# Kernel optimization log

Hardware: AMD Instinct MI355X
Metric: run time of the kernel (lower is better)

The kernel has to match this reference:

```python
import jax, jax.numpy as jnp
import numpy as np

EPS = 1e-5

def _layernorm(x, g, b):
    m = jnp.mean(x, axis=-1, keepdims=True)
    v = jnp.var(x, axis=-1, keepdims=True)
    return (x - m) * jax.lax.rsqrt(v + EPS) * g + b

def setup_inputs() -> dict:
    key = jax.random.key(0)
    ks = jax.random.split(key, 8)
    B, N, D, H = 4, 2048, 1024, 16
    F = 2 * D
    s = 0.02
    return {
        "x": jax.random.normal(ks[0], (B, N, D), jnp.float32),
        "mask": jnp.zeros((B, N, N), jnp.float32),
        "Wq": jax.random.normal(ks[1], (D, D), jnp.float32) * s,
        "Wk": jax.random.normal(ks[2], (D, D), jnp.float32) * s,
        "Wv": jax.random.normal(ks[3], (D, D), jnp.float32) * s,
        "Wc": jax.random.normal(ks[4], (D, D), jnp.float32) * s,
        "bc": jnp.zeros((D,), jnp.float32),
        "W1": jax.random.normal(ks[5], (D, F), jnp.float32) * s,
        "b1": jnp.zeros((F,), jnp.float32),
        "W2": jax.random.normal(ks[6], (F, D), jnp.float32) * s,
        "b2": jnp.zeros((D,), jnp.float32),
        "g1": jnp.ones((D,), jnp.float32),
        "be1": jnp.zeros((D,), jnp.float32),
        "g2": jnp.ones((D,), jnp.float32),
        "be2": jnp.zeros((D,), jnp.float32),
    }

def reference(x, mask, Wq, Wk, Wv, Wc, bc, W1, b1, W2, b2, g1, be1, g2, be2):
    B, N, D = x.shape
    H = 16
    Dh = D // H
    scale = 1.0 / np.sqrt(Dh).astype(np.float32)
    # projections -> [B, H, N, Dh]
    def heads(t):
        return t.reshape(B, N, H, Dh).transpose(0, 2, 1, 3)
    q = heads(x @ Wq)
    k = heads(x @ Wk)
    v = heads(x @ Wv)
    score = jnp.einsum('bhnd,bhmd->bhnm', q, k) * scale + mask[:, None, :, :]
    attn = jnp.einsum('bhnm,bhmd->bhnd', jax.nn.softmax(score, axis=-1), v)
    attn = attn.transpose(0, 2, 1, 3).reshape(B, N, D)
    x = x + attn @ Wc + bc
    x = _layernorm(x, g1, be1)
    x = x + jnp.maximum(x @ W1 + b1, 0.0) @ W2 + b2
    x = _layernorm(x, g2, be2)
    return x
```

## Files before the change

kernel.cpp:

```cpp
#include <hip/hip_runtime.h>
#include <hip/hip_bf16.h>


#define DEV __device__ __forceinline__

using s16x8  = __attribute__((ext_vector_type(8))) short;
using f32x4  = __attribute__((ext_vector_type(4))) float;

DEV unsigned short f2bf(float f) {
  unsigned u = __float_as_uint(f);
  u += 0x7fffu + ((u >> 16) & 1u);
  return (unsigned short)(u >> 16);
}
DEV unsigned cvt_pk_bf16(float lo, float hi) {
  unsigned r;
  asm("v_cvt_pk_bf16_f32 %0, %1, %2" : "=v"(r) : "v"(lo), "v"(hi));
  return r;
}
DEV float bf2f(unsigned short b) { return __uint_as_float((unsigned)b << 16); }

typedef __attribute__((address_space(3))) unsigned lds_u32_t;
typedef const __attribute__((address_space(1))) unsigned glb_u32_t;

DEV void gld_lds16(const void* g, void* l) {
  __builtin_amdgcn_global_load_lds((glb_u32_t*)g, (lds_u32_t*)l, 16, 0, 0);
}

template<int RELU>
__global__ __launch_bounds__(512, 2)
void gemm8p(const unsigned short* __restrict__ A, const unsigned short* __restrict__ Bt,
            unsigned short* __restrict__ Cb, const float* __restrict__ bias,
            int M, int N, int K)
{
  __shared__ unsigned short Sh[2][2][256 * 64];
  const int tid = threadIdx.x;
  const int w = tid >> 6, lane = tid & 63;
  const int g = lane >> 4, q = lane & 15;
  const int wr = w >> 2, wc = w & 3;

  const int nwg  = gridDim.x * gridDim.y;
  const int flat = blockIdx.y * gridDim.x + blockIdx.x;
  const int rm   = (flat & 7) * (nwg >> 3) + (flat >> 3);
  const int m0 = (rm / gridDim.x) * 256, n0 = (rm % gridDim.x) * 256;

  f32x4 acc[8][4] = {};

  const int srow = w * 8 + (lane >> 3);
  const int scol = ((lane & 7) ^ (lane >> 3)) * 8;
  const unsigned short* Ag = A  + (size_t)(m0 + srow) * K + scol;
  const unsigned short* Bg = Bt + (size_t)(n0 + srow) * K + scol;

  auto STG = [&](const unsigned short* Gb, int buf, int ab, int half, int kt) {
    const unsigned short* gs = Gb + (size_t)(half * 128) * K + kt * 64;
    unsigned short* ls = &Sh[buf][ab][(half * 128 + w * 8) * 64];
    gld_lds16(gs, ls);
    gld_lds16(gs + (size_t)64 * K, ls + 64 * 64);
  };
  auto LDA = [&](int buf, int mq, s16x8 af[4][2]) {
#pragma unroll
    for (int mm = 0; mm < 4; ++mm) {
      const unsigned short* rp = &Sh[buf][0][(wr * 128 + mq * 64 + mm * 16 + q) * 64];
#pragma unroll
      for (int kk = 0; kk < 2; ++kk)
        af[mm][kk] = *(const s16x8*)(rp + (((kk * 4 + g) ^ (q & 7)) * 8));
    }
  };
  auto LDB = [&](int buf, int nq, s16x8 bf[2][2]) {
#pragma unroll
    for (int nn = 0; nn < 2; ++nn) {
      const unsigned short* rp = &Sh[buf][1][(wc * 64 + nq * 32 + nn * 16 + q) * 64];
#pragma unroll
      for (int kk = 0; kk < 2; ++kk)
        bf[nn][kk] = *(const s16x8*)(rp + (((kk * 4 + g) ^ (q & 7)) * 8));
    }
  };
  auto MQ = [&](int mq, int nq, const s16x8 af[4][2], const s16x8 bf[2][2]) {
    __builtin_amdgcn_s_setprio(1);
#pragma unroll
    for (int kk = 0; kk < 2; ++kk)
#pragma unroll
      for (int mm = 0; mm < 4; ++mm)
#pragma unroll
        for (int nn = 0; nn < 2; ++nn)
          acc[mq * 4 + mm][nq * 2 + nn] = __builtin_amdgcn_mfma_f32_16x16x32_bf16(
              af[mm][kk], bf[nn][kk], acc[mq * 4 + mm][nq * 2 + nn], 0, 0, 0);
    __builtin_amdgcn_s_setprio(0);
  };
  auto BAR = [&]() { __builtin_amdgcn_sched_barrier(0); __builtin_amdgcn_s_barrier(); };

  STG(Ag, 0, 0, 0, 0); STG(Ag, 0, 0, 1, 0);
  STG(Bg, 0, 1, 0, 0); STG(Bg, 0, 1, 1, 0);

  const int NKT = K >> 6;
  s16x8 af[4][2], bf0[2][2], bf1[2][2];
#pragma unroll 1
  for (int kt = 0; kt < NKT; ++kt) {
    const int b = kt & 1, sb = b ^ 1, kn = kt + 1;
    const bool stg = (kn < NKT);
    if (stg) { STG(Ag, sb, 0, 0, kn); asm volatile("s_waitcnt vmcnt(2)" ::: "memory"); }
    else     {                        asm volatile("s_waitcnt vmcnt(0)" ::: "memory"); }
    BAR();
    LDA(b, 0, af); LDB(b, 0, bf0);
    MQ(0, 0, af, bf0);
    BAR();
    if (stg) STG(Ag, sb, 0, 1, kn);
    LDB(b, 1, bf1);
    MQ(0, 1, af, bf1);
    BAR();
    if (stg) STG(Bg, sb, 1, 0, kn);
    LDA(b, 1, af);
    MQ(1, 0, af, bf0);
    BAR();
    if (stg) STG(Bg, sb, 1, 1, kn);
    MQ(1, 1, af, bf1);
    BAR();
  }

#pragma unroll
  for (int n = 0; n < 4; ++n) {
    const int col = n0 + wc * 64 + n * 16 + q;
    const float bv = bias ? bias[col] : 0.0f;
#pragma unroll
    for (int m = 0; m < 8; ++m) {
      const int row0 = m0 + wr * 128 + m * 16 + g * 4;
#pragma unroll
      for (int r = 0; r < 4; ++r) {
        float v = acc[m][n][r] + bv;
        if (RELU) v = fmaxf(v, 0.0f);
        Cb[(size_t)(row0 + r) * N + col] = f2bf(v);
      }
    }
  }
}

template<int RELU, int RESID, int OUTF, int VOUT>
__global__ __launch_bounds__(256)
void gemm_bt(const unsigned short* __restrict__ A, const unsigned short* __restrict__ Bt,
             unsigned short* __restrict__ Cb, float* __restrict__ Cf,
             const float* __restrict__ bias, const float* __restrict__ resid,
             const unsigned short* __restrict__ residb,
             unsigned short* __restrict__ vtout,
             int M, int N, int K)
{
  __shared__ unsigned short As[2][4096];
  __shared__ unsigned short Bs[2][4096];
  const int tid  = threadIdx.x;
  const int wave = tid >> 6, lane = tid & 63;
  const int g = lane >> 4, q = lane & 15;

  const int nwg  = gridDim.x * gridDim.y;
  const int flat = blockIdx.y * gridDim.x + blockIdx.x;
  const int rm   = (nwg & 7) ? flat : ((flat & 7) * (nwg >> 3) + (flat >> 3));
  const int m0 = (rm / gridDim.x) * 128, n0 = (rm % gridDim.x) * 128;
  const int wr = wave >> 1, wc = wave & 1;

  f32x4 acc[4][4] = {};

  const int i0 = wave * 512 + lane * 8;
  const int i1 = 2048 + i0;

  auto STAGE = [&](int buf, int kt) {
    gld_lds16(A  + (size_t)(m0 + (i0 >> 5)) * K + kt + (i0 & 31), As[buf] + wave * 512);
    gld_lds16(Bt + (size_t)(n0 + (i0 >> 5)) * K + kt + (i0 & 31), Bs[buf] + wave * 512);
    gld_lds16(A  + (size_t)(m0 + (i1 >> 5)) * K + kt + (i1 & 31), As[buf] + 2048 + wave * 512);
    gld_lds16(Bt + (size_t)(n0 + (i1 >> 5)) * K + kt + (i1 & 31), Bs[buf] + 2048 + wave * 512);
  };

  STAGE(0, 0);
  __syncthreads();
  int cur = 0;
#pragma unroll 1
  for (int kt = 0; kt < K; kt += 32) {
    if (kt + 32 < K) STAGE(cur ^ 1, kt + 32);
    s16x8 a[4], b[4];
#pragma unroll
    for (int m = 0; m < 4; ++m)
      a[m] = *(const s16x8*)(As[cur] + (wr * 64 + m * 16 + q) * 32 + g * 8);
#pragma unroll
    for (int n = 0; n < 4; ++n)
      b[n] = *(const s16x8*)(Bs[cur] + (wc * 64 + n * 16 + q) * 32 + g * 8);
    __builtin_amdgcn_s_setprio(1);
#pragma unroll
    for (int m = 0; m < 4; ++m)
#pragma unroll
      for (int n = 0; n < 4; ++n)
        acc[m][n] = __builtin_amdgcn_mfma_f32_16x16x32_bf16(a[m], b[n], acc[m][n], 0, 0, 0);
    __builtin_amdgcn_s_setprio(0);
    __syncthreads();
    cur ^= 1;
  }

#pragma unroll
  for (int n = 0; n < 4; ++n) {
    const int col = n0 + wc * 64 + n * 16 + q;
    if (VOUT && col >= 2048) {
      const int cv = col - 2048;
#pragma unroll
      for (int m = 0; m < 4; ++m) {
        const int row0 = m0 + wr * 64 + m * 16 + g * 4;
        const int bb = row0 >> 11;
        ushort4 pk;
        pk.x = f2bf(acc[m][n][0]); pk.y = f2bf(acc[m][n][1]);
        pk.z = f2bf(acc[m][n][2]); pk.w = f2bf(acc[m][n][3]);
        *(ushort4*)(vtout + ((size_t)bb * 1024 + cv) * 2048 + (row0 & 2047)) = pk;
      }
    } else {
      const float scl = (VOUT && col < 1024) ? 0.18033688011112042f : 1.0f;
      const float bv = bias ? bias[col] : 0.0f;
#pragma unroll
      for (int m = 0; m < 4; ++m) {
        const int row0 = m0 + wr * 64 + m * 16 + g * 4;
#pragma unroll
        for (int r = 0; r < 4; ++r) {
          float v = VOUT ? (acc[m][n][r] * scl) : (acc[m][n][r] + bv);
          if (RELU) v = fmaxf(v, 0.0f);
          if (RESID == 1) v += resid[(size_t)(row0 + r) * N + col];
          if (RESID == 2) v += bf2f(residb[(size_t)(row0 + r) * N + col]);
          if (OUTF) Cf[(size_t)(row0 + r) * N + col] = v;
          else      Cb[(size_t)(row0 + r) * N + col] = f2bf(v);
        }
      }
    }
  }
}

__global__ __launch_bounds__(256)
void mcast_kernel(const float* __restrict__ in, unsigned short* __restrict__ out)
{
  const size_t i = ((size_t)blockIdx.x * 256 + threadIdx.x) * 4;
  const f32x4 v = *(const f32x4*)(in + i);
  const float L2E = 1.4426950408889634f;
  uint2 pk;
  pk.x = cvt_pk_bf16(fmaf(v[0], L2E, -8.0f), fmaf(v[1], L2E, -8.0f));
  pk.y = cvt_pk_bf16(fmaf(v[2], L2E, -8.0f), fmaf(v[3], L2E, -8.0f));
  *(uint2*)(out + i) = pk;
}

__global__ __launch_bounds__(256, 4)
void attn_kernel(const unsigned short* __restrict__ qkv,
                 const unsigned short* __restrict__ vt,
                 const unsigned short* __restrict__ mkb,
                 unsigned short* __restrict__ outb)
{
  __shared__ unsigned short Ks[2][4096];
  __shared__ unsigned short Vs[2][4096];
  __shared__ unsigned short Pl[4][1024];
  const int tid = threadIdx.x, wave = tid >> 6, lane = tid & 63;
  const int g = lane >> 4, q = lane & 15;

  const int flat = blockIdx.y * 32 + blockIdx.x;
  const int rm   = (flat & 7) * 256 + (flat >> 3);
  const int qt = rm & 31, bh = rm >> 5;
  const int b = bh >> 4, h = bh & 15;
  const int qrow = qt * 64 + wave * 16;
  const size_t tok0 = (size_t)b * 2048;

  const unsigned short* Qp = qkv + (tok0 + qrow + q) * 3072 + h * 64;
  const s16x8 bq0 = *(const s16x8*)(Qp + g * 8);
  const s16x8 bq1 = *(const s16x8*)(Qp + 32 + g * 8);
  const unsigned short* Mb = mkb + ((size_t)b * 2048 + qrow + q) * 2048 + g * 4;

  const int lr = lane >> 3;
  const int sc = (lane & 7) ^ lr;
  const unsigned short* Kg = qkv + tok0 * 3072 + 1024 + h * 64
                           + (size_t)(wave * 16 + lr) * 3072 + sc * 8;
  const unsigned short* Vg = vt + ((size_t)bh * 64 + wave * 16 + lr) * 2048 + sc * 8;
  unsigned short* KsW = Ks[0] + wave * 1024;
  unsigned short* VsW = Vs[0] + wave * 1024;

  s16x8 ones;
#pragma unroll
  for (int j = 0; j < 8; ++j) ones[j] = (short)0x3F80;

  f32x4 ot[4] = {};
  f32x4 sacc = {};
  f32x4 mk0[4], mk1[4];
  char* Pw = (char*)&Pl[wave][0];

  gld_lds16(Kg,            KsW);
  gld_lds16(Kg + 8 * 3072, KsW + 512);
  gld_lds16(Vg,            VsW);
  gld_lds16(Vg + 8 * 2048, VsW + 512);
#pragma unroll
  for (int m2 = 0; m2 < 4; ++m2) {
    const uint2 u = *(const uint2*)(Mb + m2 * 16);
    mk0[m2][0] = __uint_as_float(u.x << 16);
    mk0[m2][1] = __uint_as_float(u.x & 0xffff0000u);
    mk0[m2][2] = __uint_as_float(u.y << 16);
    mk0[m2][3] = __uint_as_float(u.y & 0xffff0000u);
  }
  __syncthreads();

#define ATTN_TILE(BUF, MKC, MKN, STG)                                          \
  {                                                                            \
    uint2 mu[4];                                                               \
    if (STG) {                                                                 \
      Kg += 64 * 3072; Vg += 64; Mb += 64;                                     \
      gld_lds16(Kg,            KsW + (BUF ^ 1) * 4096);                        \
      gld_lds16(Kg + 8 * 3072, KsW + (BUF ^ 1) * 4096 + 512);                  \
      gld_lds16(Vg,            VsW + (BUF ^ 1) * 4096);                        \
      gld_lds16(Vg + 8 * 2048, VsW + (BUF ^ 1) * 4096 + 512);                  \
      mu[0] = *(const uint2*)(Mb);      mu[1] = *(const uint2*)(Mb + 16);      \
      mu[2] = *(const uint2*)(Mb + 32); mu[3] = *(const uint2*)(Mb + 48);      \
    }                                                                          \
    f32x4 st[4];                                                               \
    _Pragma("unroll")                                                          \
    for (int m2 = 0; m2 < 4; ++m2) st[m2] = MKC[m2];                           \
    __builtin_amdgcn_s_setprio(1);                                             \
    _Pragma("unroll")                                                          \
    for (int m2 = 0; m2 < 4; ++m2) {                                           \
      const unsigned short* kp = Ks[BUF] + (m2 * 16 + q) * 64;                 \
      const s16x8 ak0 = *(const s16x8*)(kp + ((g       ^ (q & 7)) * 8));       \
      const s16x8 ak1 = *(const s16x8*)(kp + (((g + 4) ^ (q & 7)) * 8));       \
      st[m2] = __builtin_amdgcn_mfma_f32_16x16x32_bf16(ak0, bq0, st[m2], 0, 0, 0); \
      st[m2] = __builtin_amdgcn_mfma_f32_16x16x32_bf16(ak1, bq1, st[m2], 0, 0, 0); \
    }                                                                          \
    __builtin_amdgcn_s_setprio(0);                                             \
    _Pragma("unroll")                                                          \
    for (int m2 = 0; m2 < 4; ++m2) {                                           \
      st[m2][0] = exp2f(st[m2][0]); st[m2][1] = exp2f(st[m2][1]);              \
      st[m2][2] = exp2f(st[m2][2]); st[m2][3] = exp2f(st[m2][3]);              \
      const int bir  = m2 * 32 + g * 8;                                        \
      const int addr = q * 128 + (((bir >> 4) ^ (q & 7)) << 4) + (bir & 15);   \
      uint2 pk;                                                                \
      pk.x = cvt_pk_bf16(st[m2][0], st[m2][1]);                                \
      pk.y = cvt_pk_bf16(st[m2][2], st[m2][3]);                                \
      *(uint2*)(Pw + addr) = pk;                                               \
    }                                                                          \
    __builtin_amdgcn_s_setprio(1);                                             \
    _Pragma("unroll")                                                          \
    for (int kb = 0; kb < 2; ++kb) {                                           \
      const int blk = (kb * 4 + g) ^ (q & 7);                                  \
      const s16x8 pb = *(const s16x8*)(Pw + q * 128 + blk * 16);               \
      sacc = __builtin_amdgcn_mfma_f32_16x16x32_bf16(ones, pb, sacc, 0, 0, 0); \
      _Pragma("unroll")                                                        \
      for (int mm = 0; mm < 4; ++mm) {                                         \
        const s16x8 av = *(const s16x8*)(Vs[BUF] + (mm * 16 + q) * 64 + blk * 8); \
        ot[mm] = __builtin_amdgcn_mfma_f32_16x16x32_bf16(av, pb, ot[mm], 0, 0, 0); \
      }                                                                        \
    }                                                                          \
    __builtin_amdgcn_s_setprio(0);                                             \
    if (STG) {                                                                 \
      _Pragma("unroll")                                                        \
      for (int m2 = 0; m2 < 4; ++m2) {                                         \
        MKN[m2][0] = __uint_as_float(mu[m2].x << 16);                          \
        MKN[m2][1] = __uint_as_float(mu[m2].x & 0xffff0000u);                  \
        MKN[m2][2] = __uint_as_float(mu[m2].y << 16);                          \
        MKN[m2][3] = __uint_as_float(mu[m2].y & 0xffff0000u);                  \
      }                                                                        \
    }                                                                          \
    __syncthreads();                                                           \
  }

#pragma unroll 1
  for (int tt = 0; tt < 16; ++tt) {
    ATTN_TILE(0, mk0, mk1, true);
    ATTN_TILE(1, mk1, mk0, (tt < 15));
  }
#undef ATTN_TILE

  const float inv = 1.0f / sacc[0];
#pragma unroll
  for (int mm = 0; mm < 4; ++mm) {
    const int bir  = mm * 32 + g * 8;
    const int addr = q * 128 + (((bir >> 4) ^ (q & 7)) << 4) + (bir & 15);
    uint2 pk;
    pk.x = cvt_pk_bf16(ot[mm][0] * inv, ot[mm][1] * inv);
    pk.y = cvt_pk_bf16(ot[mm][2] * inv, ot[mm][3] * inv);
    *(uint2*)(Pw + addr) = pk;
  }
#pragma unroll
  for (int p = 0; p < 2; ++p) {
    const int c  = p * 64 + lane;
    const int qq = c >> 3, cc = c & 7;
    const int blk = cc ^ (qq & 7);
    const s16x8 vv = *(const s16x8*)(Pw + qq * 128 + blk * 16);
    *(s16x8*)(outb + (tok0 + qrow + qq) * 1024 + h * 64 + cc * 8) = vv;
  }
}

template<int INBF>
__global__ __launch_bounds__(256)
void ln_kernel(const float* __restrict__ inf, const unsigned short* __restrict__ inb,
               float* __restrict__ outf, unsigned short* __restrict__ outb,
               const float* __restrict__ gam, const float* __restrict__ bet)
{
  __shared__ float red[8];
  const int row = blockIdx.x, tid = threadIdx.x;
  f32x4 v;
  if (INBF) {
    const uint2 u = *(const uint2*)(inb + (size_t)row * 1024 + tid * 4);
    v[0] = __uint_as_float(u.x << 16); v[1] = __uint_as_float(u.x & 0xffff0000u);
    v[2] = __uint_as_float(u.y << 16); v[3] = __uint_as_float(u.y & 0xffff0000u);
  } else {
    v = *(const f32x4*)(inf + (size_t)row * 1024 + tid * 4);
  }
  float s  = v[0] + v[1] + v[2] + v[3];
  float ss = v[0]*v[0] + v[1]*v[1] + v[2]*v[2] + v[3]*v[3];
#pragma unroll
  for (int o = 1; o < 64; o <<= 1) { s += __shfl_xor(s, o); ss += __shfl_xor(ss, o); }
  if ((tid & 63) == 0) { red[tid >> 6] = s; red[4 + (tid >> 6)] = ss; }
  __syncthreads();
  s  = red[0] + red[1] + red[2] + red[3];
  ss = red[4] + red[5] + red[6] + red[7];
  const float mean = s * (1.0f / 1024.0f);
  const float var  = ss * (1.0f / 1024.0f) - mean * mean;
  const float rstd = rsqrtf(var + 1e-5f);
  const f32x4 gm = *(const f32x4*)(gam + tid * 4);
  const f32x4 bt = *(const f32x4*)(bet + tid * 4);
  f32x4 o;
#pragma unroll
  for (int j = 0; j < 4; ++j) o[j] = (v[j] - mean) * rstd * gm[j] + bt[j];
  if (outf) *(f32x4*)(outf + (size_t)row * 1024 + tid * 4) = o;
  if (outb) {
    uint2 pk; pk.x = cvt_pk_bf16(o[0], o[1]); pk.y = cvt_pk_bf16(o[2], o[3]);
    *(uint2*)(outb + (size_t)row * 1024 + tid * 4) = pk;
  }
}

__global__ __launch_bounds__(256)
void tcast_kernel(const float* __restrict__ in, unsigned short* __restrict__ out, int R, int C)
{
  __shared__ float t[32][33];
  const int tx = threadIdx.x & 31, ty = threadIdx.x >> 5;
  const int c0 = blockIdx.x * 32, r0 = blockIdx.y * 32;
#pragma unroll
  for (int k = 0; k < 4; ++k)
    t[ty + k * 8][tx] = in[(size_t)(r0 + ty + k * 8) * C + c0 + tx];
  __syncthreads();
#pragma unroll
  for (int k = 0; k < 4; ++k)
    out[(size_t)(c0 + ty + k * 8) * R + r0 + tx] = f2bf(t[tx][ty + k * 8]);
}

__global__ __launch_bounds__(256)
void cast_x_kernel(const float* __restrict__ in, unsigned short* __restrict__ out)
{
  const size_t i = ((size_t)blockIdx.x * 256 + threadIdx.x) * 4;
  const f32x4 v = *(const f32x4*)(in + i);
  uint2 pk; pk.x = cvt_pk_bf16(v[0], v[1]); pk.y = cvt_pk_bf16(v[2], v[3]);
  *(uint2*)(out + i) = pk;
}

extern "C" void kernel_launch(void* const* d_in, const int* in_sizes, int n_in,
                              void* d_out, int out_size, void* d_ws, size_t ws_size,
                              hipStream_t stream)
{
  (void)in_sizes; (void)n_in; (void)out_size; (void)ws_size;
  const float* x   = (const float*)d_in[0];
  const float* msk = (const float*)d_in[1];
  const float* Wq  = (const float*)d_in[2];
  const float* Wk  = (const float*)d_in[3];
  const float* Wv  = (const float*)d_in[4];
  const float* Wc  = (const float*)d_in[5];
  const float* bc  = (const float*)d_in[6];
  const float* W1  = (const float*)d_in[7];
  const float* b1  = (const float*)d_in[8];
  const float* W2  = (const float*)d_in[9];
  const float* b2  = (const float*)d_in[10];
  const float* g1  = (const float*)d_in[11];
  const float* be1 = (const float*)d_in[12];
  const float* g2  = (const float*)d_in[13];
  const float* be2 = (const float*)d_in[14];
  float* out = (float*)d_out;
  char* ws = (char*)d_ws;
  const size_t MB = 1u << 20;
  unsigned short* xb    = (unsigned short*)(ws + 0 * MB);
  unsigned short* wqkvt = (unsigned short*)(ws + 16 * MB);
  unsigned short* wct   = (unsigned short*)(ws + 22 * MB);
  unsigned short* w1t   = (unsigned short*)(ws + 24 * MB);
  unsigned short* w2t   = (unsigned short*)(ws + 28 * MB);
  unsigned short* qkv   = (unsigned short*)(ws + 32 * MB);
  unsigned short* vt    = (unsigned short*)(ws + 80 * MB);
  unsigned short* attnb = (unsigned short*)(ws + 96 * MB);
  unsigned short* mkb   = (unsigned short*)(ws + 112 * MB);
  unsigned short* y1b   = (unsigned short*)(ws + 112 * MB);
  unsigned short* h1b   = (unsigned short*)(ws + 128 * MB);
  unsigned short* midb  = (unsigned short*)(ws + 32 * MB);
  unsigned short* z2b   = (unsigned short*)(ws + 64 * MB);

  cast_x_kernel<<<8192, 256, 0, stream>>>(x, xb);
  mcast_kernel<<<16384, 256, 0, stream>>>(msk, mkb);
  tcast_kernel<<<dim3(32, 32), 256, 0, stream>>>(Wq, wqkvt,               1024, 1024);
  tcast_kernel<<<dim3(32, 32), 256, 0, stream>>>(Wk, wqkvt + 1024 * 1024, 1024, 1024);
  tcast_kernel<<<dim3(32, 32), 256, 0, stream>>>(Wv, wqkvt + 2048 * 1024, 1024, 1024);
  tcast_kernel<<<dim3(32, 32), 256, 0, stream>>>(Wc, wct,                 1024, 1024);
  tcast_kernel<<<dim3(64, 32), 256, 0, stream>>>(W1, w1t,                 1024, 2048);
  tcast_kernel<<<dim3(32, 64), 256, 0, stream>>>(W2, w2t,                 2048, 1024);

  gemm_bt<0, 0, 0, 1><<<dim3(24, 64), 256, 0, stream>>>(xb, wqkvt, qkv, nullptr,
                                                        nullptr, nullptr, nullptr, vt,
                                                        8192, 3072, 1024);
  attn_kernel<<<dim3(32, 64), 256, 0, stream>>>(qkv, vt, mkb, attnb);
  gemm_bt<0, 2, 0, 0><<<dim3(8, 64), 256, 0, stream>>>(attnb, wct, y1b, nullptr,
                                                       bc, nullptr, xb, nullptr,
                                                       8192, 1024, 1024);
  ln_kernel<1><<<8192, 256, 0, stream>>>(nullptr, y1b, nullptr, h1b, g1, be1);
  gemm8p<1><<<dim3(8, 32), 512, 0, stream>>>(h1b, w1t, midb, b1, 8192, 2048, 1024);
  gemm_bt<0, 2, 0, 0><<<dim3(8, 64), 256, 0, stream>>>(midb, w2t, z2b, nullptr,
                                                       b2, nullptr, h1b, nullptr,
                                                       8192, 1024, 2048);
  ln_kernel<1><<<8192, 256, 0, stream>>>(nullptr, z2b, out, nullptr, g2, be2);
}
```

Before: 422.4 us.

## Move QKV projection to 256-tile GEMM and fuse mask conversion into attention

The QKV projection moves from the 128x128 gemm_bt kernel to the larger 256x256 gemm8p kernel, which gains a VOUT path for writing transposed V and scaling Q. The separate mask-to-bf16 cast kernel is removed. The attention kernel now reads the fp32 mask directly and applies the log2e scale and offset inline. The QK accumulator is initialised in place from the mask registers instead of a copy. This drops one launch and a 32MB intermediate write and read, but the attention kernel now reads twice the mask bytes per tile, which may raise its memory pressure.

```diff
diff --git a/kernel.cpp b/kernel.cpp
--- a/kernel.cpp
+++ b/kernel.cpp
@@ -26,11 +26,11 @@
   __builtin_amdgcn_global_load_lds((glb_u32_t*)g, (lds_u32_t*)l, 16, 0, 0);
 }
 
-template<int RELU>
+template<int RELU, int VOUT>
 __global__ __launch_bounds__(512, 2)
 void gemm8p(const unsigned short* __restrict__ A, const unsigned short* __restrict__ Bt,
             unsigned short* __restrict__ Cb, const float* __restrict__ bias,
-            int M, int N, int K)
+            unsigned short* __restrict__ vtout, int M, int N, int K)
 {
   __shared__ unsigned short Sh[2][2][256 * 64];
   const int tid = threadIdx.x;
@@ -119,85 +119,11 @@
 #pragma unroll
   for (int n = 0; n < 4; ++n) {
     const int col = n0 + wc * 64 + n * 16 + q;
-    const float bv = bias ? bias[col] : 0.0f;
-#pragma unroll
-    for (int m = 0; m < 8; ++m) {
-      const int row0 = m0 + wr * 128 + m * 16 + g * 4;
-#pragma unroll
-      for (int r = 0; r < 4; ++r) {
-        float v = acc[m][n][r] + bv;
-        if (RELU) v = fmaxf(v, 0.0f);
-        Cb[(size_t)(row0 + r) * N + col] = f2bf(v);
-      }
-    }
-  }
-}
-
-template<int RELU, int RESID, int OUTF, int VOUT>
-__global__ __launch_bounds__(256)
-void gemm_bt(const unsigned short* __restrict__ A, const unsigned short* __restrict__ Bt,
-             unsigned short* __restrict__ Cb, float* __restrict__ Cf,
-             const float* __restrict__ bias, const float* __restrict__ resid,
-             const unsigned short* __restrict__ residb,
-             unsigned short* __restrict__ vtout,
-             int M, int N, int K)
-{
-  __shared__ unsigned short As[2][4096];
-  __shared__ unsigned short Bs[2][4096];
-  const int tid  = threadIdx.x;
-  const int wave = tid >> 6, lane = tid & 63;
-  const int g = lane >> 4, q = lane & 15;
-
-  const int nwg  = gridDim.x * gridDim.y;
-  const int flat = blockIdx.y * gridDim.x + blockIdx.x;
-  const int rm   = (nwg & 7) ? flat : ((flat & 7) * (nwg >> 3) + (flat >> 3));
-  const int m0 = (rm / gridDim.x) * 128, n0 = (rm % gridDim.x) * 128;
-  const int wr = wave >> 1, wc = wave & 1;
-
-  f32x4 acc[4][4] = {};
-
-  const int i0 = wave * 512 + lane * 8;
-  const int i1 = 2048 + i0;
-
-  auto STAGE = [&](int buf, int kt) {
-    gld_lds16(A  + (size_t)(m0 + (i0 >> 5)) * K + kt + (i0 & 31), As[buf] + wave * 512);
-    gld_lds16(Bt + (size_t)(n0 + (i0 >> 5)) * K + kt + (i0 & 31), Bs[buf] + wave * 512);
-    gld_lds16(A  + (size_t)(m0 + (i1 >> 5)) * K + kt + (i1 & 31), As[buf] + 2048 + wave * 512);
-    gld_lds16(Bt + (size_t)(n0 + (i1 >> 5)) * K + kt + (i1 & 31), Bs[buf] + 2048 + wave * 512);
-  };
-
-  STAGE(0, 0);
-  __syncthreads();
-  int cur = 0;
-#pragma unroll 1
-  for (int kt = 0; kt < K; kt += 32) {
-    if (kt + 32 < K) STAGE(cur ^ 1, kt + 32);
-    s16x8 a[4], b[4];
-#pragma unroll
-    for (int m = 0; m < 4; ++m)
-      a[m] = *(const s16x8*)(As[cur] + (wr * 64 + m * 16 + q) * 32 + g * 8);
-#pragma unroll
-    for (int n = 0; n < 4; ++n)
-      b[n] = *(const s16x8*)(Bs[cur] + (wc * 64 + n * 16 + q) * 32 + g * 8);
-    __builtin_amdgcn_s_setprio(1);
-#pragma unroll
-    for (int m = 0; m < 4; ++m)
-#pragma unroll
-      for (int n = 0; n < 4; ++n)
-        acc[m][n] = __builtin_amdgcn_mfma_f32_16x16x32_bf16(a[m], b[n], acc[m][n], 0, 0, 0);
-    __builtin_amdgcn_s_setprio(0);
-    __syncthreads();
-    cur ^= 1;
-  }
-
-#pragma unroll
-  for (int n = 0; n < 4; ++n) {
-    const int col = n0 + wc * 64 + n * 16 + q;
     if (VOUT && col >= 2048) {
       const int cv = col - 2048;
 #pragma unroll
-      for (int m = 0; m < 4; ++m) {
-        const int row0 = m0 + wr * 64 + m * 16 + g * 4;
+      for (int m = 0; m < 8; ++m) {
+        const int row0 = m0 + wr * 128 + m * 16 + g * 4;
         const int bb = row0 >> 11;
         ushort4 pk;
         pk.x = f2bf(acc[m][n][0]); pk.y = f2bf(acc[m][n][1]);
@@ -208,38 +134,99 @@
       const float scl = (VOUT && col < 1024) ? 0.18033688011112042f : 1.0f;
       const float bv = bias ? bias[col] : 0.0f;
 #pragma unroll
-      for (int m = 0; m < 4; ++m) {
-        const int row0 = m0 + wr * 64 + m * 16 + g * 4;
+      for (int m = 0; m < 8; ++m) {
+        const int row0 = m0 + wr * 128 + m * 16 + g * 4;
 #pragma unroll
         for (int r = 0; r < 4; ++r) {
-          float v = VOUT ? (acc[m][n][r] * scl) : (acc[m][n][r] + bv);
+          float v = acc[m][n][r] * scl + bv;
           if (RELU) v = fmaxf(v, 0.0f);
-          if (RESID == 1) v += resid[(size_t)(row0 + r) * N + col];
-          if (RESID == 2) v += bf2f(residb[(size_t)(row0 + r) * N + col]);
-          if (OUTF) Cf[(size_t)(row0 + r) * N + col] = v;
-          else      Cb[(size_t)(row0 + r) * N + col] = f2bf(v);
+          Cb[(size_t)(row0 + r) * N + col] = f2bf(v);
         }
       }
     }
   }
 }
 
+template<int RELU, int RESID, int OUTF>
 __global__ __launch_bounds__(256)
-void mcast_kernel(const float* __restrict__ in, unsigned short* __restrict__ out)
-{
-  const size_t i = ((size_t)blockIdx.x * 256 + threadIdx.x) * 4;
-  const f32x4 v = *(const f32x4*)(in + i);
-  const float L2E = 1.4426950408889634f;
-  uint2 pk;
-  pk.x = cvt_pk_bf16(fmaf(v[0], L2E, -8.0f), fmaf(v[1], L2E, -8.0f));
-  pk.y = cvt_pk_bf16(fmaf(v[2], L2E, -8.0f), fmaf(v[3], L2E, -8.0f));
-  *(uint2*)(out + i) = pk;
+void gemm_bt(const unsigned short* __restrict__ A, const unsigned short* __restrict__ Bt,
+             unsigned short* __restrict__ Cb, float* __restrict__ Cf,
+             const float* __restrict__ bias, const float* __restrict__ resid,
+             const unsigned short* __restrict__ residb,
+             int M, int N, int K)
+{
+  __shared__ unsigned short As[2][4096];
+  __shared__ unsigned short Bs[2][4096];
+  const int tid  = threadIdx.x;
+  const int wave = tid >> 6, lane = tid & 63;
+  const int g = lane >> 4, q = lane & 15;
+
+  const int nwg  = gridDim.x * gridDim.y;
+  const int flat = blockIdx.y * gridDim.x + blockIdx.x;
+  const int rm   = (nwg & 7) ? flat : ((flat & 7) * (nwg >> 3) + (flat >> 3));
+  const int m0 = (rm / gridDim.x) * 128, n0 = (rm % gridDim.x) * 128;
+  const int wr = wave >> 1, wc = wave & 1;
+
+  f32x4 acc[4][4] = {};
+
+  const int i0 = wave * 512 + lane * 8;
+  const int i1 = 2048 + i0;
+
+  auto STAGE = [&](int buf, int kt) {
+    gld_lds16(A  + (size_t)(m0 + (i0 >> 5)) * K + kt + (i0 & 31), As[buf] + wave * 512);
+    gld_lds16(Bt + (size_t)(n0 + (i0 >> 5)) * K + kt + (i0 & 31), Bs[buf] + wave * 512);
+    gld_lds16(A  + (size_t)(m0 + (i1 >> 5)) * K + kt + (i1 & 31), As[buf] + 2048 + wave * 512);
+    gld_lds16(Bt + (size_t)(n0 + (i1 >> 5)) * K + kt + (i1 & 31), Bs[buf] + 2048 + wave * 512);
+  };
+
+  STAGE(0, 0);
+  __syncthreads();
+  int cur = 0;
+#pragma unroll 1
+  for (int kt = 0; kt < K; kt += 32) {
+    if (kt + 32 < K) STAGE(cur ^ 1, kt + 32);
+    s16x8 a[4], b[4];
+#pragma unroll
+    for (int m = 0; m < 4; ++m)
+      a[m] = *(const s16x8*)(As[cur] + (wr * 64 + m * 16 + q) * 32 + g * 8);
+#pragma unroll
+    for (int n = 0; n < 4; ++n)
+      b[n] = *(const s16x8*)(Bs[cur] + (wc * 64 + n * 16 + q) * 32 + g * 8);
+    __builtin_amdgcn_s_setprio(1);
+#pragma unroll
+    for (int m = 0; m < 4; ++m)
+#pragma unroll
+      for (int n = 0; n < 4; ++n)
+        acc[m][n] = __builtin_amdgcn_mfma_f32_16x16x32_bf16(a[m], b[n], acc[m][n], 0, 0, 0);
+    __builtin_amdgcn_s_setprio(0);
+    __syncthreads();
+    cur ^= 1;
+  }
+
+#pragma unroll
+  for (int n = 0; n < 4; ++n) {
+    const int col = n0 + wc * 64 + n * 16 + q;
+    const float bv = bias ? bias[col] : 0.0f;
+#pragma unroll
+    for (int m = 0; m < 4; ++m) {
+      const int row0 = m0 + wr * 64 + m * 16 + g * 4;
+#pragma unroll
+      for (int r = 0; r < 4; ++r) {
+        float v = acc[m][n][r] + bv;
+        if (RELU) v = fmaxf(v, 0.0f);
+        if (RESID == 1) v += resid[(size_t)(row0 + r) * N + col];
+        if (RESID == 2) v += bf2f(residb[(size_t)(row0 + r) * N + col]);
+        if (OUTF) Cf[(size_t)(row0 + r) * N + col] = v;
+        else      Cb[(size_t)(row0 + r) * N + col] = f2bf(v);
+      }
+    }
+  }
 }
 
 __global__ __launch_bounds__(256, 4)
 void attn_kernel(const unsigned short* __restrict__ qkv,
                  const unsigned short* __restrict__ vt,
-                 const unsigned short* __restrict__ mkb,
+                 const float* __restrict__ mask,
                  unsigned short* __restrict__ outb)
 {
   __shared__ unsigned short Ks[2][4096];
@@ -258,7 +245,7 @@
   const unsigned short* Qp = qkv + (tok0 + qrow + q) * 3072 + h * 64;
   const s16x8 bq0 = *(const s16x8*)(Qp + g * 8);
   const s16x8 bq1 = *(const s16x8*)(Qp + 32 + g * 8);
-  const unsigned short* Mb = mkb + ((size_t)b * 2048 + qrow + q) * 2048 + g * 4;
+  const float* Mp = mask + ((size_t)b * 2048 + qrow + q) * 2048 + g * 4;
 
   const int lr = lane >> 3;
   const int sc = (lane & 7) ^ lr;
@@ -276,6 +263,7 @@
   f32x4 sacc = {};
   f32x4 mk0[4], mk1[4];
   char* Pw = (char*)&Pl[wave][0];
+  const float L2E = 1.4426950408889634f;
 
   gld_lds16(Kg,            KsW);
   gld_lds16(Kg + 8 * 3072, KsW + 512);
@@ -283,48 +271,43 @@
   gld_lds16(Vg + 8 * 2048, VsW + 512);
 #pragma unroll
   for (int m2 = 0; m2 < 4; ++m2) {
-    const uint2 u = *(const uint2*)(Mb + m2 * 16);
-    mk0[m2][0] = __uint_as_float(u.x << 16);
-    mk0[m2][1] = __uint_as_float(u.x & 0xffff0000u);
-    mk0[m2][2] = __uint_as_float(u.y << 16);
-    mk0[m2][3] = __uint_as_float(u.y & 0xffff0000u);
+    const f32x4 r = *(const f32x4*)(Mp + m2 * 16);
+#pragma unroll
+    for (int i = 0; i < 4; ++i) mk0[m2][i] = fmaf(r[i], L2E, -8.0f);
   }
   __syncthreads();
 
 #define ATTN_TILE(BUF, MKC, MKN, STG)                                          \
   {                                                                            \
-    uint2 mu[4];                                                               \
+    f32x4 mu[4];                                                               \
     if (STG) {                                                                 \
-      Kg += 64 * 3072; Vg += 64; Mb += 64;                                     \
+      Kg += 64 * 3072; Vg += 64; Mp += 64;                                     \
       gld_lds16(Kg,            KsW + (BUF ^ 1) * 4096);                        \
       gld_lds16(Kg + 8 * 3072, KsW + (BUF ^ 1) * 4096 + 512);                  \
       gld_lds16(Vg,            VsW + (BUF ^ 1) * 4096);                        \
       gld_lds16(Vg + 8 * 2048, VsW + (BUF ^ 1) * 4096 + 512);                  \
-      mu[0] = *(const uint2*)(Mb);      mu[1] = *(const uint2*)(Mb + 16);      \
-      mu[2] = *(const uint2*)(Mb + 32); mu[3] = *(const uint2*)(Mb + 48);      \
+      mu[0] = *(const f32x4*)(Mp);      mu[1] = *(const f32x4*)(Mp + 16);      \
+      mu[2] = *(const f32x4*)(Mp + 32); mu[3] = *(const f32x4*)(Mp + 48);      \
     }                                                                          \
-    f32x4 st[4];                                                               \
-    _Pragma("unroll")                                                          \
-    for (int m2 = 0; m2 < 4; ++m2) st[m2] = MKC[m2];                           \
     __builtin_amdgcn_s_setprio(1);                                             \
     _Pragma("unroll")                                                          \
     for (int m2 = 0; m2 < 4; ++m2) {                                           \
       const unsigned short* kp = Ks[BUF] + (m2 * 16 + q) * 64;                 \
       const s16x8 ak0 = *(const s16x8*)(kp + ((g       ^ (q & 7)) * 8));       \
       const s16x8 ak1 = *(const s16x8*)(kp + (((g + 4) ^ (q & 7)) * 8));       \
-      st[m2] = __builtin_amdgcn_mfma_f32_16x16x32_bf16(ak0, bq0, st[m2], 0, 0, 0); \
-      st[m2] = __builtin_amdgcn_mfma_f32_16x16x32_bf16(ak1, bq1, st[m2], 0, 0, 0); \
+      MKC[m2] = __builtin_amdgcn_mfma_f32_16x16x32_bf16(ak0, bq0, MKC[m2], 0, 0, 0); \
+      MKC[m2] = __builtin_amdgcn_mfma_f32_16x16x32_bf16(ak1, bq1, MKC[m2], 0, 0, 0); \
     }                                                                          \
     __builtin_amdgcn_s_setprio(0);                                             \
     _Pragma("unroll")                                                          \
     for (int m2 = 0; m2 < 4; ++m2) {                                           \
-      st[m2][0] = exp2f(st[m2][0]); st[m2][1] = exp2f(st[m2][1]);              \
-      st[m2][2] = exp2f(st[m2][2]); st[m2][3] = exp2f(st[m2][3]);              \
+      MKC[m2][0] = exp2f(MKC[m2][0]); MKC[m2][1] = exp2f(MKC[m2][1]);          \
+      MKC[m2][2] = exp2f(MKC[m2][2]); MKC[m2][3] = exp2f(MKC[m2][3]);          \
       const int bir  = m2 * 32 + g * 8;                                        \
       const int addr = q * 128 + (((bir >> 4) ^ (q & 7)) << 4) + (bir & 15);   \
       uint2 pk;                                                                \
-      pk.x = cvt_pk_bf16(st[m2][0], st[m2][1]);                                \
-      pk.y = cvt_pk_bf16(st[m2][2], st[m2][3]);                                \
+      pk.x = cvt_pk_bf16(MKC[m2][0], MKC[m2][1]);                              \
+      pk.y = cvt_pk_bf16(MKC[m2][2], MKC[m2][3]);                              \
       *(uint2*)(Pw + addr) = pk;                                               \
     }                                                                          \
     __builtin_amdgcn_s_setprio(1);                                             \
@@ -343,10 +326,10 @@
     if (STG) {                                                                 \
       _Pragma("unroll")                                                        \
       for (int m2 = 0; m2 < 4; ++m2) {                                         \
-        MKN[m2][0] = __uint_as_float(mu[m2].x << 16);                          \
-        MKN[m2][1] = __uint_as_float(mu[m2].x & 0xffff0000u);                  \
-        MKN[m2][2] = __uint_as_float(mu[m2].y << 16);                          \
-        MKN[m2][3] = __uint_as_float(mu[m2].y & 0xffff0000u);                  \
+        MKN[m2][0] = fmaf(mu[m2][0], L2E, -8.0f);                              \
+        MKN[m2][1] = fmaf(mu[m2][1], L2E, -8.0f);                              \
+        MKN[m2][2] = fmaf(mu[m2][2], L2E, -8.0f);                              \
+        MKN[m2][3] = fmaf(mu[m2][3], L2E, -8.0f);                              \
       }                                                                        \
     }                                                                          \
     __syncthreads();                                                           \
@@ -473,14 +456,12 @@
   unsigned short* qkv   = (unsigned short*)(ws + 32 * MB);
   unsigned short* vt    = (unsigned short*)(ws + 80 * MB);
   unsigned short* attnb = (unsigned short*)(ws + 96 * MB);
-  unsigned short* mkb   = (unsigned short*)(ws + 112 * MB);
   unsigned short* y1b   = (unsigned short*)(ws + 112 * MB);
   unsigned short* h1b   = (unsigned short*)(ws + 128 * MB);
   unsigned short* midb  = (unsigned short*)(ws + 32 * MB);
   unsigned short* z2b   = (unsigned short*)(ws + 64 * MB);
 
   cast_x_kernel<<<8192, 256, 0, stream>>>(x, xb);
-  mcast_kernel<<<16384, 256, 0, stream>>>(msk, mkb);
   tcast_kernel<<<dim3(32, 32), 256, 0, stream>>>(Wq, wqkvt,               1024, 1024);
   tcast_kernel<<<dim3(32, 32), 256, 0, stream>>>(Wk, wqkvt + 1024 * 1024, 1024, 1024);
   tcast_kernel<<<dim3(32, 32), 256, 0, stream>>>(Wv, wqkvt + 2048 * 1024, 1024, 1024);
@@ -488,17 +469,15 @@
   tcast_kernel<<<dim3(64, 32), 256, 0, stream>>>(W1, w1t,                 1024, 2048);
   tcast_kernel<<<dim3(32, 64), 256, 0, stream>>>(W2, w2t,                 2048, 1024);
 
-  gemm_bt<0, 0, 0, 1><<<dim3(24, 64), 256, 0, stream>>>(xb, wqkvt, qkv, nullptr,
-                                                        nullptr, nullptr, nullptr, vt,
-                                                        8192, 3072, 1024);
-  attn_kernel<<<dim3(32, 64), 256, 0, stream>>>(qkv, vt, mkb, attnb);
-  gemm_bt<0, 2, 0, 0><<<dim3(8, 64), 256, 0, stream>>>(attnb, wct, y1b, nullptr,
-                                                       bc, nullptr, xb, nullptr,
-                                                       8192, 1024, 1024);
+  gemm8p<0, 1><<<dim3(12, 32), 512, 0, stream>>>(xb, wqkvt, qkv, nullptr, vt,
+                                                 8192, 3072, 1024);
+  attn_kernel<<<dim3(32, 64), 256, 0, stream>>>(qkv, vt, msk, attnb);
+  gemm_bt<0, 2, 0><<<dim3(8, 64), 256, 0, stream>>>(attnb, wct, y1b, nullptr,
+                                                    bc, nullptr, xb, 8192, 1024, 1024);
   ln_kernel<1><<<8192, 256, 0, stream>>>(nullptr, y1b, nullptr, h1b, g1, be1);
-  gemm8p<1><<<dim3(8, 32), 512, 0, stream>>>(h1b, w1t, midb, b1, 8192, 2048, 1024);
-  gemm_bt<0, 2, 0, 0><<<dim3(8, 64), 256, 0, stream>>>(midb, w2t, z2b, nullptr,
-                                                       b2, nullptr, h1b, nullptr,
-                                                       8192, 1024, 2048);
+  gemm8p<1, 0><<<dim3(8, 32), 512, 0, stream>>>(h1b, w1t, midb, b1, nullptr,
+                                                8192, 2048, 1024);
+  gemm_bt<0, 2, 0><<<dim3(8, 64), 256, 0, stream>>>(midb, w2t, z2b, nullptr,
+                                                    b2, nullptr, h1b, 8192, 1024, 2048);
   ln_kernel<1><<<8192, 256, 0, stream>>>(nullptr, z2b, out, nullptr, g2, be2);
 }
```

Measured after the change: 418.2 us. No clear change (-1.0%).
